# Performance work log

Hardware: AMD Instinct MI355X
Metric: run time of the kernel (lower is better)

Reference implementation:

```python
import jax, jax.numpy as jnp
import numpy as np

N = 50000
E = 800000
IN_DIM = 128
OUT_DIM = 128


def setup_inputs() -> dict:
    key = jax.random.key(0)
    k_x, k_e, k_w, k_b = jax.random.split(key, 4)
    x = jax.random.normal(k_x, (N, IN_DIM), dtype=jnp.float32)
    edge_index = jax.random.randint(k_e, (2, E), 0, N, dtype=jnp.int64)
    # nn.Linear(in_dim, out_dim): W [out, in], b [out], uniform(-1/sqrt(in), 1/sqrt(in))
    bound = 1.0 / np.sqrt(IN_DIM)
    W = jax.random.uniform(k_w, (OUT_DIM, IN_DIM), jnp.float32, -bound, bound)
    b = jax.random.uniform(k_b, (OUT_DIM,), jnp.float32, -bound, bound)
    return {"x": x, "edge_index": edge_index, "W": W, "b": b}


def reference(x, edge_index, W, b):
    row, col = edge_index[0], edge_index[1]
    n = x.shape[0]
    # degree of destination nodes (count of incoming edges per node)
    deg = jax.ops.segment_sum(jnp.ones_like(col, dtype=x.dtype), col, num_segments=n)
    deg_inv = jnp.where(deg > 0, 1.0 / deg, 0.0)  # 1/0 -> 0, as in torch code
    norm = deg_inv[col]  # [E]
    msg = x[row] * norm[:, None]  # [E, in_dim]
    out = jax.ops.segment_sum(msg, col, num_segments=n)  # mean of neighbors
    h = x - out  # high-pass filter
    return jax.nn.relu(h @ W.T + b)
```

## Files before the change

### kernel.cpp

```cpp
#include <hip/hip_runtime.h>
#include <hip/hip_bf16.h>

#define DIM 128
#define NB 512
#define BCAP 2048
#define PART_CH 2048
#define SPLIT 4

typedef __attribute__((ext_vector_type(8))) short bf16x8;
typedef __attribute__((ext_vector_type(4))) float f32x4;

struct PartS { int lh[NB]; int lbase[NB]; };
struct GemmS { unsigned short Wt[DIM][DIM + 8]; unsigned short xs[64][DIM + 8]; };

__global__ __launch_bounds__(256) void k_partgemm(const int* __restrict__ ei,
                                                  const float* __restrict__ x,
                                                  const float* __restrict__ W,
                                                  int* __restrict__ gcur,
                                                  unsigned* __restrict__ ebuf,
                                                  unsigned short* __restrict__ yb,
                                                  int nE, int cpb, int PB, int nN) {
    __shared__ union { PartS p; GemmS g; } sm;
    int t = threadIdx.x;

    if ((int)blockIdx.x >= PB) {
        int n0 = ((int)blockIdx.x - PB) * 64;
        #define B16(f) (__hip_bfloat16_raw(__float2bfloat16(f)).x)
        for (int i = t; i < DIM * DIM / 4; i += 256) {
            float4 v = ((const float4*)W)[i];
            int o = i >> 5, k = (i & 31) * 4;
            sm.g.Wt[o][k] = B16(v.x); sm.g.Wt[o][k + 1] = B16(v.y);
            sm.g.Wt[o][k + 2] = B16(v.z); sm.g.Wt[o][k + 3] = B16(v.w);
        }
        for (int i = t; i < 64 * DIM / 4; i += 256) {
            int r = i >> 5, k = (i & 31) * 4;
            int n = n0 + r;
            float4 v = make_float4(0.f, 0.f, 0.f, 0.f);
            if (n < nN) v = ((const float4*)x)[(size_t)n * 32 + (i & 31)];
            sm.g.xs[r][k] = B16(v.x); sm.g.xs[r][k + 1] = B16(v.y);
            sm.g.xs[r][k + 2] = B16(v.z); sm.g.xs[r][k + 3] = B16(v.w);
        }
        #undef B16
        __syncthreads();

        int wv = t >> 6, l = t & 63;
        int lr = l & 15, lg = l >> 4;
        int row0 = wv * 16;

        bf16x8 af[4];
        #pragma unroll
        for (int kt = 0; kt < 4; ++kt)
            af[kt] = *(const bf16x8*)&sm.g.xs[row0 + lr][kt * 32 + lg * 8];

        #pragma unroll
        for (int ot = 0; ot < 8; ++ot) {
            f32x4 acc = {0.f, 0.f, 0.f, 0.f};
            #pragma unroll
            for (int kt = 0; kt < 4; ++kt) {
                bf16x8 bf = *(const bf16x8*)&sm.g.Wt[ot * 16 + lr][kt * 32 + lg * 8];
                acc = __builtin_amdgcn_mfma_f32_16x16x32_bf16(af[kt], bf, acc, 0, 0, 0);
            }
            int o = ot * 16 + lr;
            #pragma unroll
            for (int j = 0; j < 4; ++j) {
                int n = n0 + row0 + lg * 4 + j;
                if (n < nN)
                    yb[(size_t)n * DIM + o] = __hip_bfloat16_raw(__float2bfloat16(acc[j])).x;
            }
        }
        return;
    }

    int base = blockIdx.x * PART_CH;
    for (int i = t; i < NB; i += 256) sm.p.lh[i] = 0;
    __syncthreads();
    unsigned pk[8];
    int bk[8], rk[8];
    #pragma unroll
    for (int k = 0; k < 8; ++k) {
        int e = base + k * 256 + t;
        if (e < nE) {
            int row = ei[e];
            int col = ei[nE + e];
            int b = (int)((unsigned)col / (unsigned)cpb);
            bk[k] = b;
            pk[k] = ((unsigned)row << 16) | (unsigned)(col - b * cpb);
            rk[k] = atomicAdd(&sm.p.lh[b], 1);
        } else bk[k] = -1;
    }
    __syncthreads();
    for (int i = t; i < NB; i += 256) {
        int c = sm.p.lh[i];
        sm.p.lbase[i] = c ? atomicAdd(&gcur[i], c) : 0;
    }
    __syncthreads();
    #pragma unroll
    for (int k = 0; k < 8; ++k) {
        if (bk[k] >= 0) {
            int pos = sm.p.lbase[bk[k]] + rk[k];
            if (pos < BCAP) ebuf[(size_t)bk[k] * BCAP + pos] = pk[k];
        }
    }
}

__global__ __launch_bounds__(256) void k_gather(const unsigned short* __restrict__ yb,
                                                const unsigned* __restrict__ ebuf,
                                                const int* __restrict__ gcur,
                                                const float* __restrict__ bias,
                                                float* __restrict__ out,
                                                int nN, int cpb) {
    __shared__ unsigned short rowlist[BCAP];
    __shared__ int chist[128];
    __shared__ int cstart[128];
    __shared__ int part[256];
    int b = blockIdx.x / SPLIT;
    int q = blockIdx.x % SPLIT;
    int t = threadIdx.x;
    int c0 = b * cpb;
    int ncols = min(cpb, nN - c0);
    if (ncols <= 0) return;
    int CQ = (cpb + SPLIT - 1) / SPLIT;
    int mylo = q * CQ;
    int myhi = min(mylo + CQ, ncols);
    if (mylo >= ncols) return;
    int ne = min(gcur[b], BCAP);

    if (t < 128) chist[t] = 0;
    __syncthreads();

    unsigned ed[8];
    int rk[8];
    #pragma unroll
    for (int k = 0; k < 8; ++k) {
        int i = k * 256 + t;
        ed[k] = (i < ne) ? ebuf[(size_t)b * BCAP + i] : 0xFFFFFFFFu;
        if (ed[k] != 0xFFFFFFFFu) rk[k] = atomicAdd(&chist[ed[k] & 0xFFFF], 1);
    }
    __syncthreads();

    int v = (t < 128) ? chist[t] : 0;
    part[t] = v;
    __syncthreads();
    for (int off = 1; off < 128; off <<= 1) {
        int add = (t >= off) ? part[t - off] : 0;
        __syncthreads();
        part[t] += add;
        __syncthreads();
    }
    if (t < 128) cstart[t] = part[t] - v;
    __syncthreads();

    #pragma unroll
    for (int k = 0; k < 8; ++k) {
        if (ed[k] != 0xFFFFFFFFu)
            rowlist[cstart[ed[k] & 0xFFFF] + rk[k]] = (unsigned short)(ed[k] >> 16);
    }
    __syncthreads();

    int l = t & 31;
    const ushort4* yb4 = (const ushort4*)yb;
    float4 bv = ((const float4*)bias)[l];
    #define BF2F(u) __uint_as_float(((unsigned)(u)) << 16)
    #define ACC(vv) { a0 += BF2F(vv.x); a1 += BF2F(vv.y); a2 += BF2F(vv.z); a3 += BF2F(vv.w); }
    for (int cc = mylo + (t >> 5); cc < myhi; cc += 8) {
        int cdeg = chist[cc];
        int sb = cstart[cc];
        float a0 = 0.f, a1 = 0.f, a2 = 0.f, a3 = 0.f;
        int j = 0;
        for (; j + 8 <= cdeg; j += 8) {
            int r0 = rowlist[sb + j],     r1 = rowlist[sb + j + 1];
            int r2 = rowlist[sb + j + 2], r3 = rowlist[sb + j + 3];
            int r4 = rowlist[sb + j + 4], r5 = rowlist[sb + j + 5];
            int r6 = rowlist[sb + j + 6], r7 = rowlist[sb + j + 7];
            ushort4 v0 = yb4[(size_t)r0 * 32 + l];
            ushort4 v1 = yb4[(size_t)r1 * 32 + l];
            ushort4 v2 = yb4[(size_t)r2 * 32 + l];
            ushort4 v3 = yb4[(size_t)r3 * 32 + l];
            ushort4 v4 = yb4[(size_t)r4 * 32 + l];
            ushort4 v5 = yb4[(size_t)r5 * 32 + l];
            ushort4 v6 = yb4[(size_t)r6 * 32 + l];
            ushort4 v7 = yb4[(size_t)r7 * 32 + l];
            ACC(v0) ACC(v1) ACC(v2) ACC(v3) ACC(v4) ACC(v5) ACC(v6) ACC(v7)
        }
        for (; j < cdeg; ++j) {
            ushort4 vv = yb4[(size_t)rowlist[sb + j] * 32 + l];
            ACC(vv)
        }
        float dinv = cdeg > 0 ? 1.0f / (float)cdeg : 0.0f;
        int n = c0 + cc;
        ushort4 sv = yb4[(size_t)n * 32 + l];
        float4 o;
        o.x = fmaxf(BF2F(sv.x) - dinv * a0 + bv.x, 0.f);
        o.y = fmaxf(BF2F(sv.y) - dinv * a1 + bv.y, 0.f);
        o.z = fmaxf(BF2F(sv.z) - dinv * a2 + bv.z, 0.f);
        o.w = fmaxf(BF2F(sv.w) - dinv * a3 + bv.w, 0.f);
        ((float4*)out)[(size_t)n * 32 + l] = o;
    }
    #undef ACC
    #undef BF2F
}

extern "C" void kernel_launch(void* const* d_in, const int* in_sizes, int n_in,
                              void* d_out, int out_size, void* d_ws, size_t ws_size,
                              hipStream_t stream) {
    const float* x = (const float*)d_in[0];
    const int* ei = (const int*)d_in[1];
    const float* W = (const float*)d_in[2];
    const float* b = (const float*)d_in[3];
    float* out = (float*)d_out;

    int nN = in_sizes[0] / DIM;
    int nE = in_sizes[1] / 2;

    int* gcur = (int*)d_ws;
    unsigned* ebuf = (unsigned*)(gcur + NB);
    unsigned short* yb = (unsigned short*)(ebuf + (size_t)NB * BCAP);

    int cpb = (nN + NB - 1) / NB;
    int nbuckets = (nN + cpb - 1) / cpb;

    hipMemsetAsync(gcur, 0, NB * sizeof(int), stream);

    int PB = (nE + PART_CH - 1) / PART_CH;
    int GB = (nN + 63) / 64;
    k_partgemm<<<PB + GB, 256, 0, stream>>>(ei, x, W, gcur, ebuf, yb, nE, cpb, PB, nN);

    k_gather<<<nbuckets * SPLIT, 256, 0, stream>>>(yb, ebuf, gcur, b, out, nN, cpb);
}
```

Baseline: 75.90 us.

## Split GEMM output into feature planes and pin planes to XCDs with persistent queues

The bf16 GEMM output is stored as four 32-feature planes instead of row-major 128-wide rows. The gather kernel becomes persistent: it reads the hardware XCC ID, and each pair of XCDs serves one feature plane, split into two halves of the buckets, pulling work from a per-XCD atomic counter. The aim is to keep each XCD's random-row gathers inside a smaller working set that can stay resident in that XCD's L2, instead of every XCD touching the whole feature matrix. Edge-buffer loads and output stores are marked nontemporal. The cost is that each bucket's histogram and sort is rebuilt once per plane, and correctness depends on the 8-XCD assumption and on every XCD receiving at least one block.

Result: slower. 112.5 us (+48.2%).

```diff
diff --git a/kernel.cpp b/kernel.cpp
--- a/kernel.cpp
+++ b/kernel.cpp
@@ -5,7 +5,7 @@
 #define NB 512
 #define BCAP 2048
 #define PART_CH 2048
-#define SPLIT 4
+#define NXCD 8
 
 typedef __attribute__((ext_vector_type(8))) short bf16x8;
 typedef __attribute__((ext_vector_type(4))) float f32x4;
@@ -18,10 +18,11 @@
                                                   const float* __restrict__ W,
                                                   int* __restrict__ gcur,
                                                   unsigned* __restrict__ ebuf,
-                                                  unsigned short* __restrict__ yb,
+                                                  unsigned short* __restrict__ ybq,
                                                   int nE, int cpb, int PB, int nN) {
     __shared__ union { PartS p; GemmS g; } sm;
     int t = threadIdx.x;
+    int nN32 = nN * 32;
 
     if ((int)blockIdx.x >= PB) {
         int n0 = ((int)blockIdx.x - PB) * 64;
@@ -40,7 +41,6 @@
             sm.g.xs[r][k] = B16(v.x); sm.g.xs[r][k + 1] = B16(v.y);
             sm.g.xs[r][k + 2] = B16(v.z); sm.g.xs[r][k + 3] = B16(v.w);
         }
-        #undef B16
         __syncthreads();
 
         int wv = t >> 6, l = t & 63;
@@ -61,13 +61,15 @@
                 acc = __builtin_amdgcn_mfma_f32_16x16x32_bf16(af[kt], bf, acc, 0, 0, 0);
             }
             int o = ot * 16 + lr;
+            int plane = o >> 5, od = o & 31;
             #pragma unroll
             for (int j = 0; j < 4; ++j) {
                 int n = n0 + row0 + lg * 4 + j;
                 if (n < nN)
-                    yb[(size_t)n * DIM + o] = __hip_bfloat16_raw(__float2bfloat16(acc[j])).x;
-            }
-        }
+                    ybq[(size_t)plane * nN32 + (size_t)n * 32 + od] = B16(acc[j]);
+            }
+        }
+        #undef B16
         return;
     }
 
@@ -103,101 +105,117 @@
     }
 }
 
-__global__ __launch_bounds__(256) void k_gather(const unsigned short* __restrict__ yb,
+__global__ __launch_bounds__(256) void k_gather(const unsigned short* __restrict__ ybq,
                                                 const unsigned* __restrict__ ebuf,
                                                 const int* __restrict__ gcur,
+                                                int* __restrict__ xcur,
                                                 const float* __restrict__ bias,
                                                 float* __restrict__ out,
-                                                int nN, int cpb) {
+                                                int nN, int cpb, int nbuckets) {
+    unsigned xcd;
+    asm volatile("s_getreg_b32 %0, hwreg(HW_REG_XCC_ID)" : "=s"(xcd));
+    xcd &= (NXCD - 1);
+    int qr = xcd >> 1;
+    int half = xcd & 1;
+    int items0 = min(nbuckets, 256);
+    int items = half ? (nbuckets - items0) : items0;
+
+    __shared__ int s_item;
     __shared__ unsigned short rowlist[BCAP];
     __shared__ int chist[128];
     __shared__ int cstart[128];
     __shared__ int part[256];
-    int b = blockIdx.x / SPLIT;
-    int q = blockIdx.x % SPLIT;
+
     int t = threadIdx.x;
-    int c0 = b * cpb;
-    int ncols = min(cpb, nN - c0);
-    if (ncols <= 0) return;
-    int CQ = (cpb + SPLIT - 1) / SPLIT;
-    int mylo = q * CQ;
-    int myhi = min(mylo + CQ, ncols);
-    if (mylo >= ncols) return;
-    int ne = min(gcur[b], BCAP);
-
-    if (t < 128) chist[t] = 0;
-    __syncthreads();
-
-    unsigned ed[8];
-    int rk[8];
-    #pragma unroll
-    for (int k = 0; k < 8; ++k) {
-        int i = k * 256 + t;
-        ed[k] = (i < ne) ? ebuf[(size_t)b * BCAP + i] : 0xFFFFFFFFu;
-        if (ed[k] != 0xFFFFFFFFu) rk[k] = atomicAdd(&chist[ed[k] & 0xFFFF], 1);
-    }
-    __syncthreads();
-
-    int v = (t < 128) ? chist[t] : 0;
-    part[t] = v;
-    __syncthreads();
-    for (int off = 1; off < 128; off <<= 1) {
-        int add = (t >= off) ? part[t - off] : 0;
-        __syncthreads();
-        part[t] += add;
-        __syncthreads();
-    }
-    if (t < 128) cstart[t] = part[t] - v;
-    __syncthreads();
-
-    #pragma unroll
-    for (int k = 0; k < 8; ++k) {
-        if (ed[k] != 0xFFFFFFFFu)
-            rowlist[cstart[ed[k] & 0xFFFF] + rk[k]] = (unsigned short)(ed[k] >> 16);
-    }
-    __syncthreads();
-
-    int l = t & 31;
-    const ushort4* yb4 = (const ushort4*)yb;
-    float4 bv = ((const float4*)bias)[l];
-    #define BF2F(u) __uint_as_float(((unsigned)(u)) << 16)
-    #define ACC(vv) { a0 += BF2F(vv.x); a1 += BF2F(vv.y); a2 += BF2F(vv.z); a3 += BF2F(vv.w); }
-    for (int cc = mylo + (t >> 5); cc < myhi; cc += 8) {
-        int cdeg = chist[cc];
-        int sb = cstart[cc];
-        float a0 = 0.f, a1 = 0.f, a2 = 0.f, a3 = 0.f;
-        int j = 0;
-        for (; j + 8 <= cdeg; j += 8) {
-            int r0 = rowlist[sb + j],     r1 = rowlist[sb + j + 1];
-            int r2 = rowlist[sb + j + 2], r3 = rowlist[sb + j + 3];
-            int r4 = rowlist[sb + j + 4], r5 = rowlist[sb + j + 5];
-            int r6 = rowlist[sb + j + 6], r7 = rowlist[sb + j + 7];
-            ushort4 v0 = yb4[(size_t)r0 * 32 + l];
-            ushort4 v1 = yb4[(size_t)r1 * 32 + l];
-            ushort4 v2 = yb4[(size_t)r2 * 32 + l];
-            ushort4 v3 = yb4[(size_t)r3 * 32 + l];
-            ushort4 v4 = yb4[(size_t)r4 * 32 + l];
-            ushort4 v5 = yb4[(size_t)r5 * 32 + l];
-            ushort4 v6 = yb4[(size_t)r6 * 32 + l];
-            ushort4 v7 = yb4[(size_t)r7 * 32 + l];
-            ACC(v0) ACC(v1) ACC(v2) ACC(v3) ACC(v4) ACC(v5) ACC(v6) ACC(v7)
-        }
-        for (; j < cdeg; ++j) {
-            ushort4 vv = yb4[(size_t)rowlist[sb + j] * 32 + l];
-            ACC(vv)
-        }
-        float dinv = cdeg > 0 ? 1.0f / (float)cdeg : 0.0f;
-        int n = c0 + cc;
-        ushort4 sv = yb4[(size_t)n * 32 + l];
-        float4 o;
-        o.x = fmaxf(BF2F(sv.x) - dinv * a0 + bv.x, 0.f);
-        o.y = fmaxf(BF2F(sv.y) - dinv * a1 + bv.y, 0.f);
-        o.z = fmaxf(BF2F(sv.z) - dinv * a2 + bv.z, 0.f);
-        o.w = fmaxf(BF2F(sv.w) - dinv * a3 + bv.w, 0.f);
-        ((float4*)out)[(size_t)n * 32 + l] = o;
-    }
-    #undef ACC
-    #undef BF2F
+    int nN32 = nN * 32;
+    int planeBase4 = qr * (nN >> 2) * 32;
+    const ushort4* yb4 = (const ushort4*)ybq;
+    int cg = t >> 3;
+    int l8 = t & 7;
+    float4 bv = ((const float4*)bias)[qr * 8 + l8];
+
+    for (;;) {
+        if (t == 0) s_item = atomicAdd(&xcur[xcd], 1);
+        __syncthreads();
+        int it = s_item;
+        if (it >= items) break;
+        int b = half * items0 + it;
+        int c0 = b * cpb;
+        int ncols = min(cpb, nN - c0);
+        int ne = min(gcur[b], BCAP);
+
+        if (t < 128) chist[t] = 0;
+        __syncthreads();
+
+        unsigned ed[8];
+        int rk[8];
+        #pragma unroll
+        for (int k = 0; k < 8; ++k) {
+            int i = k * 256 + t;
+            ed[k] = (i < ne) ? __builtin_nontemporal_load(&ebuf[(size_t)b * BCAP + i])
+                             : 0xFFFFFFFFu;
+            if (ed[k] != 0xFFFFFFFFu) rk[k] = atomicAdd(&chist[ed[k] & 0xFFFF], 1);
+        }
+        __syncthreads();
+
+        int v = (t < 128) ? chist[t] : 0;
+        part[t] = v;
+        __syncthreads();
+        for (int off = 1; off < 128; off <<= 1) {
+            int add = (t >= off) ? part[t - off] : 0;
+            __syncthreads();
+            part[t] += add;
+            __syncthreads();
+        }
+        if (t < 128) cstart[t] = part[t] - v;
+        __syncthreads();
+
+        #pragma unroll
+        for (int k = 0; k < 8; ++k) {
+            if (ed[k] != 0xFFFFFFFFu)
+                rowlist[cstart[ed[k] & 0xFFFF] + rk[k]] = (unsigned short)(ed[k] >> 16);
+        }
+        __syncthreads();
+
+        #define BF2F(u) __uint_as_float(((unsigned)(u)) << 16)
+        #define ACC(vv) { a0 += BF2F(vv.x); a1 += BF2F(vv.y); a2 += BF2F(vv.z); a3 += BF2F(vv.w); }
+        for (int cc = cg; cc < ncols; cc += 32) {
+            int cdeg = chist[cc];
+            int sb = cstart[cc];
+            float a0 = 0.f, a1 = 0.f, a2 = 0.f, a3 = 0.f;
+            int j = 0;
+            for (; j + 8 <= cdeg; j += 8) {
+                int r0 = rowlist[sb + j],     r1 = rowlist[sb + j + 1];
+                int r2 = rowlist[sb + j + 2], r3 = rowlist[sb + j + 3];
+                int r4 = rowlist[sb + j + 4], r5 = rowlist[sb + j + 5];
+                int r6 = rowlist[sb + j + 6], r7 = rowlist[sb + j + 7];
+                ushort4 v0 = yb4[planeBase4 + r0 * 8 + l8];
+                ushort4 v1 = yb4[planeBase4 + r1 * 8 + l8];
+                ushort4 v2 = yb4[planeBase4 + r2 * 8 + l8];
+                ushort4 v3 = yb4[planeBase4 + r3 * 8 + l8];
+                ushort4 v4 = yb4[planeBase4 + r4 * 8 + l8];
+                ushort4 v5 = yb4[planeBase4 + r5 * 8 + l8];
+                ushort4 v6 = yb4[planeBase4 + r6 * 8 + l8];
+                ushort4 v7 = yb4[planeBase4 + r7 * 8 + l8];
+                ACC(v0) ACC(v1) ACC(v2) ACC(v3) ACC(v4) ACC(v5) ACC(v6) ACC(v7)
+            }
+            for (; j < cdeg; ++j) {
+                ushort4 vv = yb4[planeBase4 + rowlist[sb + j] * 8 + l8];
+                ACC(vv)
+            }
+            float dinv = cdeg > 0 ? 1.0f / (float)cdeg : 0.0f;
+            int n = c0 + cc;
+            ushort4 sv = yb4[planeBase4 + n * 8 + l8];
+            f32x4 o;
+            o.x = fmaxf(BF2F(sv.x) - dinv * a0 + bv.x, 0.f);
+            o.y = fmaxf(BF2F(sv.y) - dinv * a1 + bv.y, 0.f);
+            o.z = fmaxf(BF2F(sv.z) - dinv * a2 + bv.z, 0.f);
+            o.w = fmaxf(BF2F(sv.w) - dinv * a3 + bv.w, 0.f);
+            __builtin_nontemporal_store(o, &((f32x4*)out)[(size_t)n * 32 + qr * 8 + l8]);
+        }
+        #undef ACC
+        #undef BF2F
+    }
 }
 
 extern "C" void kernel_launch(void* const* d_in, const int* in_sizes, int n_in,
@@ -213,17 +231,18 @@
     int nE = in_sizes[1] / 2;
 
     int* gcur = (int*)d_ws;
-    unsigned* ebuf = (unsigned*)(gcur + NB);
-    unsigned short* yb = (unsigned short*)(ebuf + (size_t)NB * BCAP);
+    int* xcur = gcur + NB;
+    unsigned* ebuf = (unsigned*)(xcur + 16);
+    unsigned short* ybq = (unsigned short*)(ebuf + (size_t)NB * BCAP);
 
     int cpb = (nN + NB - 1) / NB;
     int nbuckets = (nN + cpb - 1) / cpb;
 
-    hipMemsetAsync(gcur, 0, NB * sizeof(int), stream);
+    (void)hipMemsetAsync(gcur, 0, (NB + 16) * sizeof(int), stream);
 
     int PB = (nE + PART_CH - 1) / PART_CH;
     int GB = (nN + 63) / 64;
-    k_partgemm<<<PB + GB, 256, 0, stream>>>(ei, x, W, gcur, ebuf, yb, nE, cpb, PB, nN);
-
-    k_gather<<<nbuckets * SPLIT, 256, 0, stream>>>(yb, ebuf, gcur, b, out, nN, cpb);
+    k_partgemm<<<PB + GB, 256, 0, stream>>>(ei, x, W, gcur, ebuf, ybq, nE, cpb, PB, nN);
+
+    k_gather<<<2048, 256, 0, stream>>>(ybq, ebuf, gcur, xcur, b, out, nN, cpb, nbuckets);
 }
```
